# Optimization experiments

Hardware: AMD Instinct MI355X
Metric: run time of the kernel (lower is better)

## Reference

```python
import jax, jax.numpy as jnp
import numpy as np

N_SRC, N_TGT, N_EDGES = 100000, 50000, 1000000
S_IN, T_IN, S_OUT, T_OUT = 128, 128, 64, 64
NEG_SLOPE = 0.2


def setup_inputs() -> dict:
    key = jax.random.key(0)
    ks = jax.random.split(key, 7)
    return {
        "x_source": jax.random.normal(ks[0], (N_SRC, S_IN), jnp.float32),
        "x_target": jax.random.normal(ks[1], (N_TGT, T_IN), jnp.float32),
        "w_s": jax.random.normal(ks[2], (S_IN, T_OUT), jnp.float32) * 0.1,
        "w_t": jax.random.normal(ks[3], (T_IN, S_OUT), jnp.float32) * 0.1,
        "att_weight": jax.random.normal(ks[4], (T_OUT + S_OUT,), jnp.float32) * 0.1,
        "nbhd_values": jnp.ones((N_EDGES,), jnp.float32),
        "rows": jax.random.randint(ks[5], (N_EDGES,), 0, N_TGT, jnp.int32),  # target idx i
        "cols": jax.random.randint(ks[6], (N_EDGES,), 0, N_SRC, jnp.int32),  # source idx j
    }


def reference(x_source, x_target, w_s, w_t, att_weight, nbhd_values, rows, cols):
    n_src, n_tgt = x_source.shape[0], x_target.shape[0]
    t_out = w_s.shape[1]  # dim of s_message
    s_out = w_t.shape[1]  # dim of t_message

    s_msg = x_source @ w_s  # [n_src, t_out]
    t_msg = x_target @ w_t  # [n_tgt, s_out]

    # e_{ij} = LeakyReLU([s_msg_j || t_msg_i] . a); a = [a_s (t_out) || a_t (s_out)]
    a_s, a_t = att_weight[:t_out], att_weight[t_out:]
    # f uses permuted attention vector: [a[s_out:] || a[:s_out]] on [t_msg_j || s_msg_i]
    b_t, b_s = att_weight[s_out:], att_weight[:s_out]

    es = s_msg @ a_s  # [n_src]
    et = t_msg @ a_t  # [n_tgt]
    ft = t_msg @ b_t  # [n_tgt]
    fs = s_msg @ b_s  # [n_src]

    # s->t attention: rows are target cells (row-normalize over target rows)
    e = jax.nn.leaky_relu(es[cols] + et[rows], NEG_SLOPE)  # [E]
    e_den = jax.ops.segment_sum(e, rows, num_segments=n_tgt)
    att_st = e / e_den[rows]

    # t->s attention: transposed indices; rows are source cells
    f = jax.nn.leaky_relu(ft[rows] + fs[cols], NEG_SLOPE)  # [E]
    f_den = jax.ops.segment_sum(f, cols, num_segments=n_src)
    att_ts = f / f_den[cols]

    # Hadamard with neighborhood values, then sparse-dense aggregation
    w_st = att_st * nbhd_values  # [E]
    w_ts = att_ts * nbhd_values  # [E]

    message_on_target = jax.ops.segment_sum(w_st[:, None] * s_msg[cols], rows, num_segments=n_tgt)  # [n_tgt, t_out]
    message_on_source = jax.ops.segment_sum(w_ts[:, None] * t_msg[rows], cols, num_segments=n_src)  # [n_src, s_out]

    # update_func is None -> identity
    return message_on_source, message_on_target
```

## Files before the change

kernel.cpp:

```cpp
#include <hip/hip_runtime.h>

#define N_SRC   100000
#define N_TGT   50000
#define N_EDGES 1000000
#define NEG     0.2
#define NXCD    8
#define TPART   (N_TGT / NXCD)
#define SPART   (N_SRC / NXCD)

#define GBLK_S  1563
#define GBLK_T  782
#define GBLK    (GBLK_S + GBLK_T)
#define NHIST   640


#define XS2 65
__global__ __launch_bounds__(256) void fused_gemm_hist(
    const float* __restrict__ x_source, const float* __restrict__ x_target,
    const float* __restrict__ w_s, const float* __restrict__ w_t,
    const float* __restrict__ att,
    float* __restrict__ s_msg, float* __restrict__ t_msg,
    double* __restrict__ es_d, double* __restrict__ et_d,
    const int* __restrict__ rows, const int* __restrict__ cols,
    int* __restrict__ cnt_r, int* __restrict__ cnt_c,
    unsigned* __restrict__ packT, unsigned* __restrict__ packC)
{
    __shared__ float xs[64 * XS2];
    __shared__ double eds[4][64];
    const int tid = threadIdx.x;

    if (blockIdx.x < NHIST) {
        const int S = NHIST * 256;
        int i = blockIdx.x * 256 + tid;
        for (; i + 3 * S < N_EDGES; i += 4 * S) {
            const unsigned r0 = rows[i],         c0_ = cols[i];
            const unsigned r1 = rows[i + S],     c1_ = cols[i + S];
            const unsigned r2 = rows[i + 2 * S], c2_ = cols[i + 2 * S];
            const unsigned r3 = rows[i + 3 * S], c3_ = cols[i + 3 * S];
            const unsigned kr0 = atomicAdd(&cnt_r[r0], 1);
            const unsigned kc0 = atomicAdd(&cnt_c[c0_], 1);
            const unsigned kr1 = atomicAdd(&cnt_r[r1], 1);
            const unsigned kc1 = atomicAdd(&cnt_c[c1_], 1);
            const unsigned kr2 = atomicAdd(&cnt_r[r2], 1);
            const unsigned kc2 = atomicAdd(&cnt_c[c2_], 1);
            const unsigned kr3 = atomicAdd(&cnt_r[r3], 1);
            const unsigned kc3 = atomicAdd(&cnt_c[c3_], 1);
            packT[i]         = r0 | (kr0 << 16); packC[i]         = c0_ | (kc0 << 17);
            packT[i + S]     = r1 | (kr1 << 16); packC[i + S]     = c1_ | (kc1 << 17);
            packT[i + 2 * S] = r2 | (kr2 << 16); packC[i + 2 * S] = c2_ | (kc2 << 17);
            packT[i + 3 * S] = r3 | (kr3 << 16); packC[i + 3 * S] = c3_ | (kc3 << 17);
        }
        for (; i < N_EDGES; i += S) {
            const unsigned r = rows[i], c = cols[i];
            packT[i] = r | ((unsigned)atomicAdd(&cnt_r[r], 1) << 16);
            packC[i] = c | ((unsigned)atomicAdd(&cnt_c[c], 1) << 17);
        }
        return;
    }

    const int gi = blockIdx.x - NHIST;

    const float* x; const float* w; int att_off, nrows, bblk;
    float* msg; double* evec;
    if (gi < GBLK_S) { x = x_source; w = w_s; att_off = 0;  nrows = N_SRC;
                       msg = s_msg;  evec = es_d; bblk = gi; }
    else             { x = x_target; w = w_t; att_off = 64; nrows = N_TGT;
                       msg = t_msg;  evec = et_d; bblk = gi - GBLK_S; }

    const int lane = tid & 63;
    const int part = tid >> 6;
    const int c0   = __builtin_amdgcn_readfirstlane(part << 4);
    const int row0 = bblk * 64;
    const int row  = row0 + lane;
    const bool act = row < nrows;

    float acc[16];
    #pragma unroll
    for (int c = 0; c < 16; ++c) acc[c] = 0.f;

    const int xbase = lane * XS2;

    #pragma unroll
    for (int it = 0; it < 4; ++it) {
        const int fid = tid + it * 256;
        const int r = fid >> 4, q = fid & 15;
        if (row0 + r < nrows) {
            const float4 v = *(const float4*)(x + (size_t)(row0 + r) * 128 + 4 * q);
            float* d = &xs[r * XS2 + 4 * q];
            d[0] = v.x; d[1] = v.y; d[2] = v.z; d[3] = v.w;
        }
    }
    __syncthreads();

    float4 pre[4];
    #pragma unroll
    for (int it = 0; it < 4; ++it) {
        const int fid = tid + it * 256;
        const int r = fid >> 4, q = fid & 15;
        pre[it] = (row0 + r < nrows)
            ? *(const float4*)(x + (size_t)(row0 + r) * 128 + 64 + 4 * q)
            : make_float4(0.f, 0.f, 0.f, 0.f);
    }

    for (int kc = 0; kc < 64; kc += 16) {
        #pragma unroll
        for (int kk = 0; kk < 16; ++kk) {
            const float xk = xs[xbase + kc + kk];
            const float* wr = w + (size_t)(kc + kk) * 64 + c0;
            #pragma unroll
            for (int c = 0; c < 16; ++c)
                acc[c] = fmaf(xk, wr[c], acc[c]);
        }
    }
    __syncthreads();

    #pragma unroll
    for (int it = 0; it < 4; ++it) {
        const int fid = tid + it * 256;
        const int r = fid >> 4, q = fid & 15;
        float* d = &xs[r * XS2 + 4 * q];
        d[0] = pre[it].x; d[1] = pre[it].y; d[2] = pre[it].z; d[3] = pre[it].w;
    }
    __syncthreads();

    for (int kc = 0; kc < 64; kc += 16) {
        #pragma unroll
        for (int kk = 0; kk < 16; ++kk) {
            const float xk = xs[xbase + kc + kk];
            const float* wr = w + (size_t)(64 + kc + kk) * 64 + c0;
            #pragma unroll
            for (int c = 0; c < 16; ++c)
                acc[c] = fmaf(xk, wr[c], acc[c]);
        }
    }

    double e = 0.0;
    #pragma unroll
    for (int c = 0; c < 16; ++c)
        e += (double)acc[c] * (double)att[att_off + c0 + c];
    eds[part][lane] = e;
    __syncthreads();
    if (part == 0 && act)
        evec[row] = eds[0][lane] + eds[1][lane] + eds[2][lane] + eds[3][lane];

    if (act) {
        float* mo = msg + (size_t)row * 64 + c0;
        #pragma unroll
        for (int q = 0; q < 4; ++q)
            *(float4*)(mo + 4 * q) = *(float4*)(acc + 4 * q);
    }
}

__global__ __launch_bounds__(1024) void scan_two(
    const int* __restrict__ cnt_r, const int* __restrict__ cnt_c,
    int* __restrict__ ptr_r, int* __restrict__ ptr_c)
{
    const int n    = blockIdx.x ? N_SRC : N_TGT;
    const int* cnt = blockIdx.x ? cnt_c : cnt_r;
    int* ptr       = blockIdx.x ? ptr_c : ptr_r;
    const int tid  = threadIdx.x;
    const int lane = tid & 63, wid = tid >> 6;

    __shared__ int wsum[16];
    __shared__ int s_carry;
    if (tid == 0) s_carry = 0;
    __syncthreads();

    for (int base = 0; base < n; base += 4096) {
        const int idx = base + tid * 4;
        int4 v = make_int4(0, 0, 0, 0);
        if (idx + 3 < n) {
            v = *(const int4*)(cnt + idx);
        } else if (idx < n) {
            v.x = cnt[idx];
            if (idx + 1 < n) v.y = cnt[idx + 1];
            if (idx + 2 < n) v.z = cnt[idx + 2];
        }
        const int s = v.x + v.y + v.z + v.w;

        int p = s;
        #pragma unroll
        for (int d = 1; d < 64; d <<= 1) {
            int t = __shfl_up(p, d);
            if (lane >= d) p += t;
        }
        if (lane == 63) wsum[wid] = p;
        __syncthreads();
        if (tid == 0) {
            int a = 0;
            #pragma unroll
            for (int i = 0; i < 16; ++i) { int t = wsum[i]; wsum[i] = a; a += t; }
        }
        __syncthreads();

        int run = s_carry + wsum[wid] + (p - s);
        if (idx     < n) ptr[idx]     = run; run += v.x;
        if (idx + 1 < n) ptr[idx + 1] = run; run += v.y;
        if (idx + 2 < n) ptr[idx + 2] = run; run += v.z;
        if (idx + 3 < n) ptr[idx + 3] = run; run += v.w;

        __syncthreads();
        if (tid == 1023) s_carry = run;
        __syncthreads();
    }
    if (tid == 0) ptr[n] = s_carry;
}

__global__ __launch_bounds__(256) void scatter_part(
    const unsigned* __restrict__ packT, const unsigned* __restrict__ packC,
    const float* __restrict__ nbhd,
    const int* __restrict__ ptr_r, const int* __restrict__ ptr_c,
    unsigned long long* __restrict__ srtT, unsigned long long* __restrict__ srtS)
{
    const int xcd  = blockIdx.x & (NXCD - 1);
    const int ibx  = blockIdx.x >> 3;
    const int step = (gridDim.x >> 3) * blockDim.x;
    const unsigned lo_r = xcd * TPART, lo_c = xcd * SPART;

    int i = ibx * blockDim.x + threadIdx.x;
    for (; i + 3 * step < N_EDGES; i += 4 * step) {
        const unsigned pT0 = packT[i],            pC0 = packC[i];
        const unsigned pT1 = packT[i + step],     pC1 = packC[i + step];
        const unsigned pT2 = packT[i + 2 * step], pC2 = packC[i + 2 * step];
        const unsigned pT3 = packT[i + 3 * step], pC3 = packC[i + 3 * step];
        const float    nf0 = nbhd[i],             nf1 = nbhd[i + step];
        const float    nf2 = nbhd[i + 2 * step],  nf3 = nbhd[i + 3 * step];

        const unsigned r0 = pT0 & 0xFFFFu, kr0 = pT0 >> 16;
        const unsigned r1 = pT1 & 0xFFFFu, kr1 = pT1 >> 16;
        const unsigned r2 = pT2 & 0xFFFFu, kr2 = pT2 >> 16;
        const unsigned r3 = pT3 & 0xFFFFu, kr3 = pT3 >> 16;
        const unsigned c0 = pC0 & 0x1FFFFu, kc0 = pC0 >> 17;
        const unsigned c1 = pC1 & 0x1FFFFu, kc1 = pC1 >> 17;
        const unsigned c2 = pC2 & 0x1FFFFu, kc2 = pC2 >> 17;
        const unsigned c3 = pC3 & 0x1FFFFu, kc3 = pC3 >> 17;

        const bool mr0 = (r0 - lo_r) < TPART, mc0 = (c0 - lo_c) < SPART;
        const bool mr1 = (r1 - lo_r) < TPART, mc1 = (c1 - lo_c) < SPART;
        const bool mr2 = (r2 - lo_r) < TPART, mc2 = (c2 - lo_c) < SPART;
        const bool mr3 = (r3 - lo_r) < TPART, mc3 = (c3 - lo_c) < SPART;

        const unsigned long long nb0 = (unsigned long long)(unsigned)__float_as_int(nf0) << 32;
        const unsigned long long nb1 = (unsigned long long)(unsigned)__float_as_int(nf1) << 32;
        const unsigned long long nb2 = (unsigned long long)(unsigned)__float_as_int(nf2) << 32;
        const unsigned long long nb3 = (unsigned long long)(unsigned)__float_as_int(nf3) << 32;

        if (mr0) srtT[ptr_r[r0] + kr0] = nb0 | c0;
        if (mr1) srtT[ptr_r[r1] + kr1] = nb1 | c1;
        if (mr2) srtT[ptr_r[r2] + kr2] = nb2 | c2;
        if (mr3) srtT[ptr_r[r3] + kr3] = nb3 | c3;
        if (mc0) srtS[ptr_c[c0] + kc0] = nb0 | r0;
        if (mc1) srtS[ptr_c[c1] + kc1] = nb1 | r1;
        if (mc2) srtS[ptr_c[c2] + kc2] = nb2 | r2;
        if (mc3) srtS[ptr_c[c3] + kc3] = nb3 | r3;
    }
    for (; i < N_EDGES; i += step) {
        const unsigned pT = packT[i], pC = packC[i];
        const unsigned r = pT & 0xFFFFu,  kr = pT >> 16;
        const unsigned c = pC & 0x1FFFFu, kc = pC >> 17;
        const bool mr = (r - lo_r) < TPART;
        const bool mc = (c - lo_c) < SPART;
        if (!(mr | mc)) continue;
        const unsigned long long nb =
            (unsigned long long)(unsigned)__float_as_int(nbhd[i]) << 32;
        if (mr) srtT[ptr_r[r] + kr] = nb | c;
        if (mc) srtS[ptr_c[c] + kc] = nb | r;
    }
}

__global__ __launch_bounds__(256) void gather_both(
    const int2* __restrict__ srtT, const int* __restrict__ ptr_r,
    const float* __restrict__ s_msg, float* __restrict__ msg_tgt,
    const int2* __restrict__ srtS, const int* __restrict__ ptr_c,
    const float* __restrict__ t_msg, float* __restrict__ msg_src,
    const double* __restrict__ es_d, const double* __restrict__ et_d)
{
    const int gw   = (blockIdx.x * blockDim.x + threadIdx.x) >> 6;
    const int lane = threadIdx.x & 63;

    const int2* srt; const int* ptr; const float* min_; float* out;
    const double* other_d; double base; int row;
    if (gw < N_TGT) {
        srt = srtT; ptr = ptr_r; min_ = s_msg; out = msg_tgt;
        other_d = es_d; row = gw; base = et_d[row];
    } else {
        row = gw - N_TGT;
        if (row >= N_SRC) return;
        srt = srtS; ptr = ptr_c; min_ = t_msg; out = msg_src;
        other_d = et_d; base = es_d[row];
    }

    const int b = ptr[row], e = ptr[row + 1];
    double den = 0.0;
    float a0 = 0.f, a1 = 0.f, a2 = 0.f, a3 = 0.f;

    for (int j0 = b; j0 < e; j0 += 64) {
        const int m = e - j0;
        int oidx = 0; double v = 0.0; float wf = 0.f;
        if (lane < m) {
            const int2 pay = srt[j0 + lane];
            oidx = pay.x;
            const float nb = __int_as_float(pay.y);
            const double sv = base + other_d[oidx];
            v = (sv >= 0.0) ? sv : NEG * sv;
            wf = (float)(v * (double)nb);
        }
        den += v;

        const int cnt = m < 64 ? m : 64;
        int j = 0;
        for (; j + 7 < cnt; j += 8) {
            const int   c0_ = __shfl(oidx, j);     const float w0 = __shfl(wf, j);
            const int   c1_ = __shfl(oidx, j + 1); const float w1 = __shfl(wf, j + 1);
            const int   c2_ = __shfl(oidx, j + 2); const float w2 = __shfl(wf, j + 2);
            const int   c3_ = __shfl(oidx, j + 3); const float w3 = __shfl(wf, j + 3);
            const int   c4_ = __shfl(oidx, j + 4); const float w4 = __shfl(wf, j + 4);
            const int   c5_ = __shfl(oidx, j + 5); const float w5 = __shfl(wf, j + 5);
            const int   c6_ = __shfl(oidx, j + 6); const float w6 = __shfl(wf, j + 6);
            const int   c7_ = __shfl(oidx, j + 7); const float w7 = __shfl(wf, j + 7);
            const float m0 = min_[(size_t)c0_ * 64 + lane];
            const float m1 = min_[(size_t)c1_ * 64 + lane];
            const float m2 = min_[(size_t)c2_ * 64 + lane];
            const float m3 = min_[(size_t)c3_ * 64 + lane];
            const float m4 = min_[(size_t)c4_ * 64 + lane];
            const float m5 = min_[(size_t)c5_ * 64 + lane];
            const float m6 = min_[(size_t)c6_ * 64 + lane];
            const float m7 = min_[(size_t)c7_ * 64 + lane];
            a0 = fmaf(w0, m0, a0); a1 = fmaf(w1, m1, a1);
            a2 = fmaf(w2, m2, a2); a3 = fmaf(w3, m3, a3);
            a0 = fmaf(w4, m4, a0); a1 = fmaf(w5, m5, a1);
            a2 = fmaf(w6, m6, a2); a3 = fmaf(w7, m7, a3);
        }
        for (; j + 3 < cnt; j += 4) {
            const int   c0_ = __shfl(oidx, j);     const float w0 = __shfl(wf, j);
            const int   c1_ = __shfl(oidx, j + 1); const float w1 = __shfl(wf, j + 1);
            const int   c2_ = __shfl(oidx, j + 2); const float w2 = __shfl(wf, j + 2);
            const int   c3_ = __shfl(oidx, j + 3); const float w3 = __shfl(wf, j + 3);
            a0 = fmaf(w0, min_[(size_t)c0_ * 64 + lane], a0);
            a1 = fmaf(w1, min_[(size_t)c1_ * 64 + lane], a1);
            a2 = fmaf(w2, min_[(size_t)c2_ * 64 + lane], a2);
            a3 = fmaf(w3, min_[(size_t)c3_ * 64 + lane], a3);
        }
        for (; j < cnt; ++j) {
            const int   c = __shfl(oidx, j);
            const float w = __shfl(wf, j);
            a0 = fmaf(w, min_[(size_t)c * 64 + lane], a0);
        }
    }
    #pragma unroll
    for (int s = 32; s; s >>= 1) den += __shfl_xor(den, s);
    const double inv = (den != 0.0) ? 1.0 / den : 0.0;
    const double acc = (double)((a0 + a1) + (a2 + a3));
    out[(size_t)row * 64 + lane] = (float)(acc * inv);
}

extern "C" void kernel_launch(void* const* d_in, const int* in_sizes, int n_in,
                              void* d_out, int out_size, void* d_ws, size_t ws_size,
                              hipStream_t stream)
{
    const float* x_source = (const float*)d_in[0];
    const float* x_target = (const float*)d_in[1];
    const float* w_s      = (const float*)d_in[2];
    const float* w_t      = (const float*)d_in[3];
    const float* att      = (const float*)d_in[4];
    const float* nbhd     = (const float*)d_in[5];
    const int*   rows     = (const int*)d_in[6];
    const int*   cols     = (const int*)d_in[7];

    float* out     = (float*)d_out;
    float* msg_src = out;
    float* msg_tgt = out + (size_t)N_SRC * 64;

    char* ws = (char*)d_ws;
    float*    s_msg  = (float*)   (ws + 0);
    float*    t_msg  = (float*)   (ws + 25600000);
    double*   es_d   = (double*)  (ws + 38400000);
    double*   et_d   = (double*)  (ws + 39200000);
    int*      cnt_r  = (int*)     (ws + 39600000);
    int*      cnt_c  = (int*)     (ws + 39800000);
    int*      ptr_r  = (int*)     (ws + 40200000);
    int*      ptr_c  = (int*)     (ws + 40400004);
    unsigned* packT  = (unsigned*)(ws + 40800016);
    unsigned* packC  = (unsigned*)(ws + 44800016);
    unsigned long long* srtT = (unsigned long long*)(ws + 48800016);
    unsigned long long* srtS = (unsigned long long*)(ws + 56800016);

    hipMemsetAsync(ws + 39600000, 0, 600000, stream);

    fused_gemm_hist<<<NHIST + GBLK, 256, 0, stream>>>(
        x_source, x_target, w_s, w_t, att,
        s_msg, t_msg, es_d, et_d,
        rows, cols, cnt_r, cnt_c, packT, packC);

    scan_two<<<2, 1024, 0, stream>>>(cnt_r, cnt_c, ptr_r, ptr_c);
    scatter_part<<<2048, 256, 0, stream>>>(
        packT, packC, nbhd, ptr_r, ptr_c, srtT, srtS);

    gather_both<<<(N_TGT + N_SRC + 3) / 4, 256, 0, stream>>>(
        (const int2*)srtT, ptr_r, s_msg, msg_tgt,
        (const int2*)srtS, ptr_c, t_msg, msg_src, es_d, et_d);
}
```

Before: 279.1 us.

## Privatize edge histogram counters into eight copies to cut atomic contention

The degree histogram is split into eight private counter arrays, selected by block index modulo eight, so fewer blocks contend on the same atomic addresses. The scan kernel now sums the eight copies and writes a per-copy base offset array. The scatter uses those per-copy bases, with the copy index chosen so it matches the histogram's copy for each edge. The base arrays are kept in the output buffer as scratch until the gather overwrites it. In exchange, the memset is eight times larger, and the two-block serial scan has to read and write eight times as much data, which may dominate.

```diff
diff --git a/kernel.cpp b/kernel.cpp
--- a/kernel.cpp
+++ b/kernel.cpp
@@ -22,7 +22,7 @@
     float* __restrict__ s_msg, float* __restrict__ t_msg,
     double* __restrict__ es_d, double* __restrict__ et_d,
     const int* __restrict__ rows, const int* __restrict__ cols,
-    int* __restrict__ cnt_r, int* __restrict__ cnt_c,
+    int* __restrict__ cnt_r8, int* __restrict__ cnt_c8,
     unsigned* __restrict__ packT, unsigned* __restrict__ packC)
 {
     __shared__ float xs[64 * XS2];
@@ -30,6 +30,9 @@
     const int tid = threadIdx.x;
 
     if (blockIdx.x < NHIST) {
+        const int g = blockIdx.x & 7;
+        int* cr = cnt_r8 + (size_t)g * N_TGT;
+        int* cc = cnt_c8 + (size_t)g * N_SRC;
         const int S = NHIST * 256;
         int i = blockIdx.x * 256 + tid;
         for (; i + 3 * S < N_EDGES; i += 4 * S) {
@@ -37,14 +40,14 @@
             const unsigned r1 = rows[i + S],     c1_ = cols[i + S];
             const unsigned r2 = rows[i + 2 * S], c2_ = cols[i + 2 * S];
             const unsigned r3 = rows[i + 3 * S], c3_ = cols[i + 3 * S];
-            const unsigned kr0 = atomicAdd(&cnt_r[r0], 1);
-            const unsigned kc0 = atomicAdd(&cnt_c[c0_], 1);
-            const unsigned kr1 = atomicAdd(&cnt_r[r1], 1);
-            const unsigned kc1 = atomicAdd(&cnt_c[c1_], 1);
-            const unsigned kr2 = atomicAdd(&cnt_r[r2], 1);
-            const unsigned kc2 = atomicAdd(&cnt_c[c2_], 1);
-            const unsigned kr3 = atomicAdd(&cnt_r[r3], 1);
-            const unsigned kc3 = atomicAdd(&cnt_c[c3_], 1);
+            const unsigned kr0 = atomicAdd(&cr[r0], 1);
+            const unsigned kc0 = atomicAdd(&cc[c0_], 1);
+            const unsigned kr1 = atomicAdd(&cr[r1], 1);
+            const unsigned kc1 = atomicAdd(&cc[c1_], 1);
+            const unsigned kr2 = atomicAdd(&cr[r2], 1);
+            const unsigned kc2 = atomicAdd(&cc[c2_], 1);
+            const unsigned kr3 = atomicAdd(&cr[r3], 1);
+            const unsigned kc3 = atomicAdd(&cc[c3_], 1);
             packT[i]         = r0 | (kr0 << 16); packC[i]         = c0_ | (kc0 << 17);
             packT[i + S]     = r1 | (kr1 << 16); packC[i + S]     = c1_ | (kc1 << 17);
             packT[i + 2 * S] = r2 | (kr2 << 16); packC[i + 2 * S] = c2_ | (kc2 << 17);
@@ -52,8 +55,8 @@
         }
         for (; i < N_EDGES; i += S) {
             const unsigned r = rows[i], c = cols[i];
-            packT[i] = r | ((unsigned)atomicAdd(&cnt_r[r], 1) << 16);
-            packC[i] = c | ((unsigned)atomicAdd(&cnt_c[c], 1) << 17);
+            packT[i] = r | ((unsigned)atomicAdd(&cr[r], 1) << 16);
+            packC[i] = c | ((unsigned)atomicAdd(&cc[c], 1) << 17);
         }
         return;
     }
@@ -152,12 +155,14 @@
 }
 
 __global__ __launch_bounds__(1024) void scan_two(
-    const int* __restrict__ cnt_r, const int* __restrict__ cnt_c,
-    int* __restrict__ ptr_r, int* __restrict__ ptr_c)
+    const int* __restrict__ cnt_r8, const int* __restrict__ cnt_c8,
+    int* __restrict__ ptr_r, int* __restrict__ ptr_c,
+    int* __restrict__ base_r8, int* __restrict__ base_c8)
 {
-    const int n    = blockIdx.x ? N_SRC : N_TGT;
-    const int* cnt = blockIdx.x ? cnt_c : cnt_r;
-    int* ptr       = blockIdx.x ? ptr_c : ptr_r;
+    const int n     = blockIdx.x ? N_SRC : N_TGT;
+    const int* cnt8 = blockIdx.x ? cnt_c8 : cnt_r8;
+    int* ptr        = blockIdx.x ? ptr_c : ptr_r;
+    int* base8      = blockIdx.x ? base_c8 : base_r8;
     const int tid  = threadIdx.x;
     const int lane = tid & 63, wid = tid >> 6;
 
@@ -168,15 +173,25 @@
 
     for (int base = 0; base < n; base += 4096) {
         const int idx = base + tid * 4;
-        int4 v = make_int4(0, 0, 0, 0);
-        if (idx + 3 < n) {
-            v = *(const int4*)(cnt + idx);
-        } else if (idx < n) {
-            v.x = cnt[idx];
-            if (idx + 1 < n) v.y = cnt[idx + 1];
-            if (idx + 2 < n) v.z = cnt[idx + 2];
-        }
-        const int s = v.x + v.y + v.z + v.w;
+        int4 v[8];
+        #pragma unroll
+        for (int g = 0; g < 8; ++g) {
+            v[g] = make_int4(0, 0, 0, 0);
+            const int* cg = cnt8 + (size_t)g * n;
+            if (idx + 3 < n) {
+                v[g] = *(const int4*)(cg + idx);
+            } else if (idx < n) {
+                v[g].x = cg[idx];
+                if (idx + 1 < n) v[g].y = cg[idx + 1];
+                if (idx + 2 < n) v[g].z = cg[idx + 2];
+            }
+        }
+        int4 sv = make_int4(0, 0, 0, 0);
+        #pragma unroll
+        for (int g = 0; g < 8; ++g) {
+            sv.x += v[g].x; sv.y += v[g].y; sv.z += v[g].z; sv.w += v[g].w;
+        }
+        const int s = sv.x + sv.y + sv.z + sv.w;
 
         int p = s;
         #pragma unroll
@@ -194,10 +209,34 @@
         __syncthreads();
 
         int run = s_carry + wsum[wid] + (p - s);
-        if (idx     < n) ptr[idx]     = run; run += v.x;
-        if (idx + 1 < n) ptr[idx + 1] = run; run += v.y;
-        if (idx + 2 < n) ptr[idx + 2] = run; run += v.z;
-        if (idx + 3 < n) ptr[idx + 3] = run; run += v.w;
+        if (idx < n) {
+            ptr[idx] = run;
+            int a2 = run;
+            #pragma unroll
+            for (int g = 0; g < 8; ++g) { base8[(size_t)g * n + idx] = a2; a2 += v[g].x; }
+        }
+        run += sv.x;
+        if (idx + 1 < n) {
+            ptr[idx + 1] = run;
+            int a2 = run;
+            #pragma unroll
+            for (int g = 0; g < 8; ++g) { base8[(size_t)g * n + idx + 1] = a2; a2 += v[g].y; }
+        }
+        run += sv.y;
+        if (idx + 2 < n) {
+            ptr[idx + 2] = run;
+            int a2 = run;
+            #pragma unroll
+            for (int g = 0; g < 8; ++g) { base8[(size_t)g * n + idx + 2] = a2; a2 += v[g].z; }
+        }
+        run += sv.z;
+        if (idx + 3 < n) {
+            ptr[idx + 3] = run;
+            int a2 = run;
+            #pragma unroll
+            for (int g = 0; g < 8; ++g) { base8[(size_t)g * n + idx + 3] = a2; a2 += v[g].w; }
+        }
+        run += sv.w;
 
         __syncthreads();
         if (tid == 1023) s_carry = run;
@@ -209,13 +248,16 @@
 __global__ __launch_bounds__(256) void scatter_part(
     const unsigned* __restrict__ packT, const unsigned* __restrict__ packC,
     const float* __restrict__ nbhd,
-    const int* __restrict__ ptr_r, const int* __restrict__ ptr_c,
+    const int* __restrict__ base_r8, const int* __restrict__ base_c8,
     unsigned long long* __restrict__ srtT, unsigned long long* __restrict__ srtS)
 {
     const int xcd  = blockIdx.x & (NXCD - 1);
     const int ibx  = blockIdx.x >> 3;
     const int step = (gridDim.x >> 3) * blockDim.x;
     const unsigned lo_r = xcd * TPART, lo_c = xcd * SPART;
+    const int g = ibx & 7;
+    const int* bT = base_r8 + (size_t)g * N_TGT;
+    const int* bC = base_c8 + (size_t)g * N_SRC;
 
     int i = ibx * blockDim.x + threadIdx.x;
     for (; i + 3 * step < N_EDGES; i += 4 * step) {
@@ -245,14 +287,14 @@
         const unsigned long long nb2 = (unsigned long long)(unsigned)__float_as_int(nf2) << 32;
         const unsigned long long nb3 = (unsigned long long)(unsigned)__float_as_int(nf3) << 32;
 
-        if (mr0) srtT[ptr_r[r0] + kr0] = nb0 | c0;
-        if (mr1) srtT[ptr_r[r1] + kr1] = nb1 | c1;
-        if (mr2) srtT[ptr_r[r2] + kr2] = nb2 | c2;
-        if (mr3) srtT[ptr_r[r3] + kr3] = nb3 | c3;
-        if (mc0) srtS[ptr_c[c0] + kc0] = nb0 | r0;
-        if (mc1) srtS[ptr_c[c1] + kc1] = nb1 | r1;
-        if (mc2) srtS[ptr_c[c2] + kc2] = nb2 | r2;
-        if (mc3) srtS[ptr_c[c3] + kc3] = nb3 | r3;
+        if (mr0) srtT[bT[r0] + kr0] = nb0 | c0;
+        if (mr1) srtT[bT[r1] + kr1] = nb1 | c1;
+        if (mr2) srtT[bT[r2] + kr2] = nb2 | c2;
+        if (mr3) srtT[bT[r3] + kr3] = nb3 | c3;
+        if (mc0) srtS[bC[c0] + kc0] = nb0 | r0;
+        if (mc1) srtS[bC[c1] + kc1] = nb1 | r1;
+        if (mc2) srtS[bC[c2] + kc2] = nb2 | r2;
+        if (mc3) srtS[bC[c3] + kc3] = nb3 | r3;
     }
     for (; i < N_EDGES; i += step) {
         const unsigned pT = packT[i], pC = packC[i];
@@ -263,8 +305,8 @@
         if (!(mr | mc)) continue;
         const unsigned long long nb =
             (unsigned long long)(unsigned)__float_as_int(nbhd[i]) << 32;
-        if (mr) srtT[ptr_r[r] + kr] = nb | c;
-        if (mc) srtS[ptr_c[c] + kc] = nb | r;
+        if (mr) srtT[bT[r] + kr] = nb | c;
+        if (mc) srtS[bC[c] + kc] = nb | r;
     }
 }
 
@@ -371,30 +413,35 @@
     float* msg_src = out;
     float* msg_tgt = out + (size_t)N_SRC * 64;
 
+    int* base_r8 = (int*)d_out;
+    int* base_c8 = (int*)((char*)d_out + 1600000);
+
     char* ws = (char*)d_ws;
     float*    s_msg  = (float*)   (ws + 0);
     float*    t_msg  = (float*)   (ws + 25600000);
     double*   es_d   = (double*)  (ws + 38400000);
     double*   et_d   = (double*)  (ws + 39200000);
-    int*      cnt_r  = (int*)     (ws + 39600000);
-    int*      cnt_c  = (int*)     (ws + 39800000);
-    int*      ptr_r  = (int*)     (ws + 40200000);
-    int*      ptr_c  = (int*)     (ws + 40400004);
-    unsigned* packT  = (unsigned*)(ws + 40800016);
-    unsigned* packC  = (unsigned*)(ws + 44800016);
-    unsigned long long* srtT = (unsigned long long*)(ws + 48800016);
-    unsigned long long* srtS = (unsigned long long*)(ws + 56800016);
-
-    hipMemsetAsync(ws + 39600000, 0, 600000, stream);
+    int*      cnt_r8 = (int*)     (ws + 39600000);
+    int*      cnt_c8 = (int*)     (ws + 41200000);
+    int*      ptr_r  = (int*)     (ws + 44400000);
+    int*      ptr_c  = (int*)     (ws + 44600004);
+    unsigned* packT  = (unsigned*)(ws + 45000008);
+    unsigned* packC  = (unsigned*)(ws + 49000008);
+    unsigned long long* srtT = (unsigned long long*)(ws + 53000008);
+    unsigned long long* srtS = (unsigned long long*)(ws + 61000008);
+
+    hipMemsetAsync(ws + 39600000, 0, 4800000, stream);
 
     fused_gemm_hist<<<NHIST + GBLK, 256, 0, stream>>>(
         x_source, x_target, w_s, w_t, att,
         s_msg, t_msg, es_d, et_d,
-        rows, cols, cnt_r, cnt_c, packT, packC);
-
-    scan_two<<<2, 1024, 0, stream>>>(cnt_r, cnt_c, ptr_r, ptr_c);
+        rows, cols, cnt_r8, cnt_c8, packT, packC);
+
+    scan_two<<<2, 1024, 0, stream>>>(
+        cnt_r8, cnt_c8, ptr_r, ptr_c, base_r8, base_c8);
+
     scatter_part<<<2048, 256, 0, stream>>>(
-        packT, packC, nbhd, ptr_r, ptr_c, srtT, srtS);
+        packT, packC, nbhd, base_r8, base_c8, srtT, srtS);
 
     gather_both<<<(N_TGT + N_SRC + 3) / 4, 256, 0, stream>>>(
         (const int2*)srtT, ptr_r, s_msg, msg_tgt,
```

After: 473.8 us. 1.7x slower.
